# Kernel tuning notes

Measured on AMD Instinct MI355X. Metric: run time of the kernel, lower is better.

The kernel has to match this reference:

```python
import jax, jax.numpy as jnp
import numpy as np

B, N, D, K = 32, 1024, 64, 2


def _spatial_attention(x, w1, w2, vs, bs):
    # x: (B, N, D); matches SpatialAttention on x.unsqueeze(1) with c_in=1
    e1 = x @ w1                                   # (B, N)
    e2 = x @ w2                                   # (B, N)
    prod = e1[:, :, None] * e2[:, None, :]        # (B, N, N) outer product
    e = jnp.einsum('ij,bjk->bik', vs, jax.nn.sigmoid(prod + bs))
    return jax.nn.softmax(e, axis=-1)


def setup_inputs() -> dict:
    key = jax.random.key(0)
    ks = jax.random.split(key, 16)
    s = jnp.float32(1.0 / np.sqrt(N))  # kaiming-like scale for NxN params
    return {
        'x': jax.random.normal(ks[0], (B, N * D), jnp.float32),
        'x0': jax.random.normal(ks[1], (B, N, D), jnp.float32),
        'w': jnp.eye(D, dtype=jnp.float32) + 0.01 * jax.random.normal(ks[2], (D, D), jnp.float32),
        'd': jnp.ones((D,), jnp.float32),
        'alpha': 0.8 * jnp.ones((N,), jnp.float32),
        'f_w1': jax.random.uniform(ks[3], (D,), jnp.float32),
        'f_w2': jax.random.uniform(ks[4], (D,), jnp.float32),
        'f_vs': s * jax.random.normal(ks[5], (N, N), jnp.float32),
        'f_bs': s * jax.random.normal(ks[6], (N, N), jnp.float32),
        'g_w1': jax.random.uniform(ks[7], (D,), jnp.float32),
        'g_w2': jax.random.uniform(ks[8], (D,), jnp.float32),
        'g_vs': s * jax.random.normal(ks[9], (N, N), jnp.float32),
        'g_bs': s * jax.random.normal(ks[10], (N, N), jnp.float32),
        'conv_w': jax.random.normal(ks[11], (K,), jnp.float32) / np.sqrt(K),
        'conv_b': jnp.zeros((1,), jnp.float32),
        'adj_mx': s * jax.random.normal(ks[12], (K, N, N), jnp.float32),
    }


def reference(x, x0, w, d, alpha, f_w1, f_w2, f_vs, f_bs,
              g_w1, g_w2, g_vs, g_bs, conv_w, conv_b, adj_mx):
    xr = x.reshape(B, N, D)
    I_N = jnp.eye(N, dtype=x.dtype)

    # ---- F (drift) ----
    E = _spatial_attention(xr, f_w1, f_w2, f_vs, f_bs)      # (B, N, N)
    xe = jnp.einsum('bij,bjd->bid', E - I_N, xr)            # attention message passing
    # channel_conv(adj @ x): 1x1 conv over K Chebyshev channels == weighted sum + bias
    A_hat = adj_mx - I_N                                    # (K, N, N)
    A_mix = jnp.einsum('k,kij->ij', conv_w, A_hat)          # fold K into one (N, N)
    xa = jnp.einsum('ij,bjd->bid', A_mix, xr) + conv_b[0]
    dc = jnp.clip(d, 0.0, 1.0)
    W_hat = (w * dc) @ w.T - jnp.eye(D, dtype=x.dtype)
    xw = xr @ W_hat
    x0t = x0 * jax.nn.sigmoid(alpha)[None, :, None]
    f = jnp.tanh(xe + xa + xw + x0t).reshape(B, N * D)

    # ---- G (diffusion), uses E cached from F ----
    N_att = _spatial_attention(xr, g_w1, g_w2, g_vs, g_bs)  # (B, N, N)
    N_hat = N_att / (E + 1e-5)
    g = jnp.tanh(jnp.einsum('bij,bjd->bid', N_hat, xr)).reshape(B, N * D)

    return f, g
```

## Files before the change

kernel.cpp:

```cpp
#include <hip/hip_runtime.h>
#include <math.h>

constexpr int B_ = 32;
constexpr int N_ = 1024;
constexpr int D_ = 64;
constexpr int BCH = 16;

typedef short short8 __attribute__((ext_vector_type(8)));
typedef float f32x4 __attribute__((ext_vector_type(4)));
typedef int   int4_ __attribute__((ext_vector_type(4)));

__device__ __forceinline__ float sigf(float v) {
    return 1.0f / (1.0f + __expf(-v));
}
__device__ __forceinline__ unsigned short f2b(float f) {
    unsigned u = __float_as_uint(f);
    unsigned r = u + 0x7fffu + ((u >> 16) & 1u);
    return (unsigned short)(r >> 16);
}
__device__ __forceinline__ float b2f(unsigned int h) {
    return __uint_as_float(h << 16);
}
__device__ __forceinline__ unsigned pack4(int a, int b, int c, int d) {
    return (unsigned)(a & 255) | ((unsigned)(b & 255) << 8) |
           ((unsigned)(c & 255) << 16) | ((unsigned)(d & 255) << 24);
}

#define GLD16(gp, lp)                                                        \
    __builtin_amdgcn_global_load_lds(                                        \
        (const __attribute__((address_space(1))) unsigned int*)(const void*)(gp), \
        (__attribute__((address_space(3))) unsigned int*)(void*)(lp), 16, 0, 0)

__global__ void k_dots(const float* __restrict__ x,
                       const float* __restrict__ fw1, const float* __restrict__ fw2,
                       const float* __restrict__ gw1, const float* __restrict__ gw2,
                       const float* __restrict__ alpha,
                       float* __restrict__ e1f, float* __restrict__ e2f,
                       float* __restrict__ e1g, float* __restrict__ e2g,
                       float* __restrict__ sa)
{
    int t = blockIdx.x * blockDim.x + threadIdx.x;
    if (t < N_) sa[t] = sigf(alpha[t]);
    if (t >= B_ * N_) return;
    const float* xr = x + (size_t)t * D_;
    float s1 = 0.f, s2 = 0.f, s3 = 0.f, s4 = 0.f;
#pragma unroll 8
    for (int d = 0; d < D_; d++) {
        float v = xr[d];
        s1 += v * fw1[d];
        s2 += v * fw2[d];
        s3 += v * gw1[d];
        s4 += v * gw2[d];
    }
    e1f[t] = s1; e2f[t] = s2; e1g[t] = s3; e2g[t] = s4;
}

__global__ void k_what2_split(const float* __restrict__ w, const float* __restrict__ dvec,
                              unsigned short* __restrict__ W2h, unsigned short* __restrict__ W2l)
{
    int t = blockIdx.x * blockDim.x + threadIdx.x;
    if (t >= D_ * D_) return;
    int i = t / D_, j = t % D_;
    float s = 0.f;
    for (int q = 0; q < D_; q++) {
        float dc = fminf(fmaxf(dvec[q], 0.0f), 1.0f);
        s += w[i * D_ + q] * dc * w[j * D_ + q];
    }
    if (i == j) s -= 2.0f;
    unsigned short h = f2b(s);
    W2h[t] = h;
    W2l[t] = f2b(s - b2f(h));
}

__global__ void k_amix_split(const float* __restrict__ adj, const float* __restrict__ cw,
                             unsigned short* __restrict__ AmixH, unsigned short* __restrict__ AmixL)
{
    int t = blockIdx.x * blockDim.x + threadIdx.x;
    if (t >= N_ * N_) return;
    int i = t >> 10, j = t & (N_ - 1);
    float c0 = cw[0], c1 = cw[1];
    float v = c0 * adj[t] + c1 * adj[(size_t)N_ * N_ + t];
    if (i == j) v -= (c0 + c1);
    unsigned short h = f2b(v);
    AmixH[t] = h;
    AmixL[t] = f2b(v - b2f(h));
}

__global__ void k_zinit(unsigned* __restrict__ amaxbits)
{
    if (threadIdx.x < 2) amaxbits[threadIdx.x] = 0;
}

__global__ void k_amax(const float* __restrict__ fvs, const float* __restrict__ gvs,
                       unsigned* __restrict__ amaxbits)
{
    int fg = blockIdx.y;
    const float* src = fg ? gvs : fvs;
    int t = threadIdx.x;
    size_t base = ((size_t)blockIdx.x * 256 + t) * 16;
    float m = 0.f;
#pragma unroll
    for (int q = 0; q < 4; q++) {
        float4 v = *(const float4*)(src + base + q * 4);
        m = fmaxf(m, fmaxf(fmaxf(fabsf(v.x), fabsf(v.y)), fmaxf(fabsf(v.z), fabsf(v.w))));
    }
#pragma unroll
    for (int o = 32; o > 0; o >>= 1) m = fmaxf(m, __shfl_xor(m, o, 64));
    __shared__ float red[4];
    if ((t & 63) == 0) red[t >> 6] = m;
    __syncthreads();
    if (t == 0) {
        m = fmaxf(fmaxf(red[0], red[1]), fmaxf(red[2], red[3]));
        atomicMax(&amaxbits[fg], __float_as_uint(m));
    }
}

__launch_bounds__(256)
__global__ void k_aquant(const float* __restrict__ fvs, const float* __restrict__ gvs,
                         const float* __restrict__ amaxf,
                         signed char* __restrict__ AHf, signed char* __restrict__ ALf,
                         signed char* __restrict__ AHg, signed char* __restrict__ ALg,
                         float* __restrict__ rsumf, float* __restrict__ rsumg)
{
    int row = blockIdx.x;
    int fg  = blockIdx.y;
    const float* src = fg ? gvs : fvs;
    signed char* hp = fg ? AHg : AHf;
    signed char* lp = fg ? ALg : ALf;
    float* rs = fg ? rsumg : rsumf;
    float inv = 32512.f / amaxf[fg];
    int t = threadIdx.x;
    int j = t * 4;
    float4 v = *(const float4*)(src + (size_t)row * N_ + j);
    float a[4] = {v.x, v.y, v.z, v.w};
    int qh[4], ql[4], s = 0;
#pragma unroll
    for (int e = 0; e < 4; e++) {
        int q = __float2int_rn(a[e] * inv);
        q = min(max(q, -32512), 32512);
        int h = (q + 128) >> 8;
        qh[e] = h;
        ql[e] = q - (h << 8);
        s += q;
    }
    *(unsigned*)(hp + (size_t)row * N_ + j) = pack4(qh[0], qh[1], qh[2], qh[3]);
    *(unsigned*)(lp + (size_t)row * N_ + j) = pack4(ql[0], ql[1], ql[2], ql[3]);
#pragma unroll
    for (int o = 32; o > 0; o >>= 1) s += __shfl_xor(s, o, 64);
    __shared__ int red[4];
    if ((t & 63) == 0) red[t >> 6] = s;
    __syncthreads();
    if (t == 0) rs[row] = (float)(red[0] + red[1] + red[2] + red[3]);
}

__launch_bounds__(256)
__global__ void k_xt_split(const float* __restrict__ xc,
                           unsigned short* __restrict__ XTh, unsigned short* __restrict__ XTl)
{
    int j0 = blockIdx.x * 64;
    int bc = blockIdx.y;
    int t  = threadIdx.x;
    __shared__ float S_l[64][65];
    {
        int j = t >> 2, dc = (t & 3) * 16;
        const float* src = xc + ((size_t)bc * N_ + j0 + j) * D_ + dc;
#pragma unroll
        for (int q = 0; q < 4; q++) {
            float4 v = *(const float4*)(src + q * 4);
            S_l[j][dc + q * 4 + 0] = v.x;
            S_l[j][dc + q * 4 + 1] = v.y;
            S_l[j][dc + q * 4 + 2] = v.z;
            S_l[j][dc + q * 4 + 3] = v.w;
        }
    }
    __syncthreads();
    {
        int d = t >> 2, jc = (t & 3) * 16;
        unsigned short hs[16], ls[16];
#pragma unroll
        for (int u = 0; u < 16; u++) {
            float v = S_l[jc + u][d];
            hs[u] = f2b(v);
            ls[u] = f2b(v - b2f(hs[u]));
        }
        uint4 hv0, hv1, lv0, lv1;
        hv0.x = hs[0] | (hs[1] << 16);  hv0.y = hs[2] | (hs[3] << 16);
        hv0.z = hs[4] | (hs[5] << 16);  hv0.w = hs[6] | (hs[7] << 16);
        hv1.x = hs[8] | (hs[9] << 16);  hv1.y = hs[10] | (hs[11] << 16);
        hv1.z = hs[12] | (hs[13] << 16); hv1.w = hs[14] | (hs[15] << 16);
        lv0.x = ls[0] | (ls[1] << 16);  lv0.y = ls[2] | (ls[3] << 16);
        lv0.z = ls[4] | (ls[5] << 16);  lv0.w = ls[6] | (ls[7] << 16);
        lv1.x = ls[8] | (ls[9] << 16);  lv1.y = ls[10] | (ls[11] << 16);
        lv1.z = ls[12] | (ls[13] << 16); lv1.w = ls[14] | (ls[15] << 16);
        size_t base = ((size_t)bc * D_ + d) * N_ + j0 + jc;
        *(uint4*)(XTh + base) = hv0;  *(uint4*)(XTh + base + 8) = hv1;
        *(uint4*)(XTl + base) = lv0;  *(uint4*)(XTl + base + 8) = lv1;
    }
}

__launch_bounds__(256)
__global__ void k_sigsplit2(const float* __restrict__ fbs, const float* __restrict__ gbs,
                            const float* __restrict__ e1f_, const float* __restrict__ e2f_,
                            const float* __restrict__ e1g_, const float* __restrict__ e2g_,
                            signed char* __restrict__ SHf, signed char* __restrict__ SLf,
                            signed char* __restrict__ SHg, signed char* __restrict__ SLg)
{
    int j0 = blockIdx.x * 64;
    int k0 = blockIdx.y * 64;
    int z  = blockIdx.z;
    int b  = z & (BCH - 1);
    int fg = z / BCH;
    const float* bs = fg ? gbs : fbs;
    const float* e1 = fg ? e1g_ : e1f_;
    const float* e2 = fg ? e2g_ : e2f_;
    signed char* SH = fg ? SHg : SHf;
    signed char* SL = fg ? SLg : SLf;
    int t  = threadIdx.x;
    __shared__ float S_l[64][65];
    {
        int j  = t >> 2;
        int kc = (t & 3) * 16;
        float e1v = e1[(size_t)b * N_ + j0 + j];
#pragma unroll
        for (int q = 0; q < 4; q++) {
            float4 bsv = *(const float4*)(bs + (size_t)(j0 + j) * N_ + k0 + kc + q * 4);
            float4 e2v = *(const float4*)(e2 + (size_t)b * N_ + k0 + kc + q * 4);
            S_l[j][kc + q * 4 + 0] = sigf(fmaf(e1v, e2v.x, bsv.x));
            S_l[j][kc + q * 4 + 1] = sigf(fmaf(e1v, e2v.y, bsv.y));
            S_l[j][kc + q * 4 + 2] = sigf(fmaf(e1v, e2v.z, bsv.z));
            S_l[j][kc + q * 4 + 3] = sigf(fmaf(e1v, e2v.w, bsv.w));
        }
    }
    __syncthreads();
    {
        int k  = t >> 2;
        int jc = (t & 3) * 16;
        int hh[16], ll[16];
#pragma unroll
        for (int u = 0; u < 16; u++) {
            float v = S_l[jc + u][k];
            int q = __float2int_rn(v * 65024.f) - 32512;
            q = min(max(q, -32512), 32512);
            int h = (q + 128) >> 8;
            hh[u] = h;
            ll[u] = q - (h << 8);
        }
        uint4 H, L;
        H.x = pack4(hh[0], hh[1], hh[2], hh[3]);   H.y = pack4(hh[4], hh[5], hh[6], hh[7]);
        H.z = pack4(hh[8], hh[9], hh[10], hh[11]); H.w = pack4(hh[12], hh[13], hh[14], hh[15]);
        L.x = pack4(ll[0], ll[1], ll[2], ll[3]);   L.y = pack4(ll[4], ll[5], ll[6], ll[7]);
        L.z = pack4(ll[8], ll[9], ll[10], ll[11]); L.w = pack4(ll[12], ll[13], ll[14], ll[15]);
        size_t base = (size_t)(b * N_ + k0 + k) * N_ + j0 + jc;
        *(uint4*)(SH + base) = H;
        *(uint4*)(SL + base) = L;
    }
}

__launch_bounds__(256, 2)
__global__ void k_gemm2i(const signed char* __restrict__ AHf, const signed char* __restrict__ ALf,
                         const signed char* __restrict__ AHg, const signed char* __restrict__ ALg,
                         const signed char* __restrict__ SHf, const signed char* __restrict__ SLf,
                         const signed char* __restrict__ SHg, const signed char* __restrict__ SLg,
                         const float* __restrict__ rsumf, const float* __restrict__ rsumg,
                         const float* __restrict__ amaxf,
                         float* __restrict__ LF, float* __restrict__ LG)
{
    const int fg = blockIdx.z;
    const signed char* AH = fg ? AHg : AHf;
    const signed char* AL = fg ? ALg : ALf;
    const signed char* SH = fg ? SHg : SHf;
    const signed char* SL = fg ? SLg : SLf;
    const float* rsum = fg ? rsumg : rsumf;
    float* Lo = fg ? LG : LF;
    const float scale = amaxf[fg] * (1.0f / (32512.f * 65024.f));

    const int b  = blockIdx.y;
    const int i0 = (blockIdx.x >> 3) * 128;
    const int k0 = (blockIdx.x & 7) * 128;
    const int t    = threadIdx.x;
    const int lane = t & 63;
    const int wave = t >> 6;
    const int wr   = wave >> 1;
    const int wc   = wave & 1;
    const int quad = lane >> 4;
    const int m16  = lane & 15;

    __shared__ __align__(16) signed char lds[32768];
    signed char* AHl = lds;
    signed char* ALl = lds + 8192;
    signed char* BHl = lds + 16384;
    signed char* BLl = lds + 24576;

    const signed char* gsrc;
    signed char* ldst;
    int rowbase;
    if (wave == 0)      { gsrc = AH; ldst = AHl; rowbase = i0; }
    else if (wave == 1) { gsrc = AL; ldst = ALl; rowbase = i0; }
    else if (wave == 2) { gsrc = SH; ldst = BHl; rowbase = b * N_ + k0; }
    else                { gsrc = SL; ldst = BLl; rowbase = b * N_ + k0; }

    int4_ accm[4][4], accc[4][4];
#pragma unroll
    for (int mi = 0; mi < 4; mi++)
#pragma unroll
        for (int ni = 0; ni < 4; ni++) {
            accm[mi][ni] = (int4_){0, 0, 0, 0};
            accc[mi][ni] = (int4_){0, 0, 0, 0};
        }

    const int rr = lane >> 2;
    const int cc = lane & 3;
    const int gcq = cc ^ ((rr >> 1) & 3);
    const int rpos = (quad ^ ((m16 >> 1) & 3)) * 16;

    for (int step = 0; step < 16; step++) {
        const int jb = step * 64;
        __syncthreads();
#pragma unroll
        for (int it = 0; it < 8; it++) {
            int r = it * 16 + rr;
            const signed char* gp = gsrc + (size_t)(rowbase + r) * N_ + jb + gcq * 16;
            GLD16(gp, ldst + it * 1024);
        }
        __syncthreads();

        int4_ ah[4], al[4];
#pragma unroll
        for (int mi = 0; mi < 4; mi++) {
            int row = wr * 64 + mi * 16 + m16;
            ah[mi] = *(const int4_*)(AHl + row * 64 + rpos);
            al[mi] = *(const int4_*)(ALl + row * 64 + rpos);
        }
#pragma unroll
        for (int ni = 0; ni < 4; ni++) {
            int row = wc * 64 + ni * 16 + m16;
            int4_ bh = *(const int4_*)(BHl + row * 64 + rpos);
            int4_ bl = *(const int4_*)(BLl + row * 64 + rpos);
#pragma unroll
            for (int mi = 0; mi < 4; mi++) {
                accm[mi][ni] = __builtin_amdgcn_mfma_i32_16x16x64_i8(
                    ah[mi], bh, accm[mi][ni], 0, 0, 0);
                accc[mi][ni] = __builtin_amdgcn_mfma_i32_16x16x64_i8(
                    ah[mi], bl, accc[mi][ni], 0, 0, 0);
                accc[mi][ni] = __builtin_amdgcn_mfma_i32_16x16x64_i8(
                    al[mi], bh, accc[mi][ni], 0, 0, 0);
            }
        }
    }

#pragma unroll
    for (int mi = 0; mi < 4; mi++)
#pragma unroll
        for (int ni = 0; ni < 4; ni++) {
            int row = i0 + wr * 64 + mi * 16 + quad * 4;
            int col = k0 + wc * 64 + ni * 16 + m16;
            size_t base = ((size_t)b * N_ + row) * N_ + col;
#pragma unroll
            for (int r = 0; r < 4; r++) {
                float v = (65536.f * (float)accm[mi][ni][r] +
                           256.f * (float)accc[mi][ni][r] +
                           32512.f * rsum[row + r]) * scale;
                Lo[base + (size_t)r * N_] = v;
            }
        }
}

__launch_bounds__(256, 2)
__global__ void k_fused(const float* __restrict__ LF, const float* __restrict__ LG,
                        const unsigned short* __restrict__ AmixH, const unsigned short* __restrict__ AmixL,
                        const unsigned short* __restrict__ XTh, const unsigned short* __restrict__ XTl,
                        const unsigned short* __restrict__ W2h, const unsigned short* __restrict__ W2l,
                        const float* __restrict__ xc, const float* __restrict__ x0c,
                        const float* __restrict__ sa, const float* __restrict__ cb,
                        float* __restrict__ outf, float* __restrict__ outg)
{
    const int i0 = blockIdx.x * 32;
    const int bc = blockIdx.y;
    const int t    = threadIdx.x;
    const int lane = t & 63;
    const int wave = t >> 6;
    const int quad = lane >> 4;
    const int m16  = lane & 15;
    const int l7   = lane & 7;
    const int r_sub = lane >> 3;
    const int gc    = l7 ^ r_sub;

    __shared__ __align__(16) unsigned short lds[18432];
    unsigned short* E_l  = lds;
    unsigned short* Nh_l = lds + 2048;
    unsigned short* Nl_l = lds + 4096;
    unsigned short* Xh_l = lds + 6144;
    unsigned short* Xl_l = lds + 10240;
    unsigned short* Ah_l = lds + 14336;
    unsigned short* Al_l = lds + 16384;
    __shared__ float invf_l[32], invg_l[32];

    {
        int r  = t >> 3;
        int c0 = (t & 7) * 4;
        const float* lf = LF + ((size_t)bc * N_ + i0 + r) * N_;
        const float* lg = LG + ((size_t)bc * N_ + i0 + r) * N_;
        float sf = 0.f, sg = 0.f;
        for (int k = 0; k < 32; k++) {
            float4 a = *(const float4*)(lf + c0 + k * 32);
            float4 b = *(const float4*)(lg + c0 + k * 32);
            sf += __expf(a.x) + __expf(a.y) + __expf(a.z) + __expf(a.w);
            sg += __expf(b.x) + __expf(b.y) + __expf(b.z) + __expf(b.w);
        }
        sf += __shfl_xor(sf, 1, 64); sf += __shfl_xor(sf, 2, 64); sf += __shfl_xor(sf, 4, 64);
        sg += __shfl_xor(sg, 1, 64); sg += __shfl_xor(sg, 2, 64); sg += __shfl_xor(sg, 4, 64);
        if ((t & 7) == 0) { invf_l[r] = 1.f / sf; invg_l[r] = 1.f / sg; }
    }
    __syncthreads();

    f32x4 accf[2], accg[2];
#pragma unroll
    for (int u = 0; u < 2; u++) {
        accf[u] = (f32x4){0.f, 0.f, 0.f, 0.f};
        accg[u] = (f32x4){0.f, 0.f, 0.f, 0.f};
    }
    const int rowA = (wave & 1) * 16 + m16;
    const int cg0  = (wave >> 1) * 2;

    for (int step = 0; step < 16; step++) {
        const int jb = step * 64;
        __syncthreads();
        for (int i = 0; i < 6; i++) {
            int gi = wave * 6 + i;
            const unsigned short* gp;
            unsigned short* lp;
            if (gi < 8) {
                gp = XTh + ((size_t)bc * D_ + gi * 8 + r_sub) * N_ + jb + gc * 8;
                lp = Xh_l + gi * 512;
            } else if (gi < 16) {
                int g2 = gi - 8;
                gp = XTl + ((size_t)bc * D_ + g2 * 8 + r_sub) * N_ + jb + gc * 8;
                lp = Xl_l + g2 * 512;
            } else if (gi < 20) {
                int g2 = gi - 16;
                gp = AmixH + (size_t)(i0 + g2 * 8 + r_sub) * N_ + jb + gc * 8;
                lp = Ah_l + g2 * 512;
            } else {
                int g2 = gi - 20;
                gp = AmixL + (size_t)(i0 + g2 * 8 + r_sub) * N_ + jb + gc * 8;
                lp = Al_l + g2 * 512;
            }
            GLD16(gp, lp);
        }
        {
            int r  = t >> 3;
            int jc = (t & 7) * 8;
            const float* lf = LF + ((size_t)bc * N_ + i0 + r) * N_ + jb + jc;
            const float* lg = LG + ((size_t)bc * N_ + i0 + r) * N_ + jb + jc;
            float4 f0 = *(const float4*)lf;
            float4 f1 = *(const float4*)(lf + 4);
            float4 g0 = *(const float4*)lg;
            float4 g1 = *(const float4*)(lg + 4);
            float fa[8] = {f0.x, f0.y, f0.z, f0.w, f1.x, f1.y, f1.z, f1.w};
            float ga[8] = {g0.x, g0.y, g0.z, g0.w, g1.x, g1.y, g1.z, g1.w};
            float fi = invf_l[r], gi2 = invg_l[r];
            short8 ev, nhv, nlv;
#pragma unroll
            for (int e = 0; e < 8; e++) {
                float E = __expf(fa[e]) * fi;
                float nh = __expf(ga[e]) * gi2 / (E + 1e-5f);
                ev[e] = (short)f2b(E);
                unsigned short h = f2b(nh);
                nhv[e] = (short)h;
                nlv[e] = (short)f2b(nh - b2f(h));
            }
            int pos = (((jc >> 3) ^ (r & 7))) * 8;
            *(short8*)(E_l  + r * 64 + pos) = ev;
            *(short8*)(Nh_l + r * 64 + pos) = nhv;
            *(short8*)(Nl_l + r * 64 + pos) = nlv;
        }
        __syncthreads();
#pragma unroll
        for (int kc = 0; kc < 2; kc++) {
            const int ch = ((kc * 4 + quad) ^ l7) * 8;
            short8 e  = *(const short8*)(E_l  + rowA * 64 + ch);
            short8 ah = *(const short8*)(Ah_l + rowA * 64 + ch);
            short8 al = *(const short8*)(Al_l + rowA * 64 + ch);
            short8 nh = *(const short8*)(Nh_l + rowA * 64 + ch);
            short8 nl = *(const short8*)(Nl_l + rowA * 64 + ch);
#pragma unroll
            for (int u = 0; u < 2; u++) {
                int rowB = (cg0 + u) * 16 + m16;
                short8 bh = *(const short8*)(Xh_l + rowB * 64 + ch);
                short8 bl = *(const short8*)(Xl_l + rowB * 64 + ch);
                accf[u] = __builtin_amdgcn_mfma_f32_16x16x32_bf16(e,  bh, accf[u], 0, 0, 0);
                accf[u] = __builtin_amdgcn_mfma_f32_16x16x32_bf16(e,  bl, accf[u], 0, 0, 0);
                accf[u] = __builtin_amdgcn_mfma_f32_16x16x32_bf16(ah, bh, accf[u], 0, 0, 0);
                accf[u] = __builtin_amdgcn_mfma_f32_16x16x32_bf16(ah, bl, accf[u], 0, 0, 0);
                accf[u] = __builtin_amdgcn_mfma_f32_16x16x32_bf16(al, bh, accf[u], 0, 0, 0);
                accg[u] = __builtin_amdgcn_mfma_f32_16x16x32_bf16(nh, bh, accg[u], 0, 0, 0);
                accg[u] = __builtin_amdgcn_mfma_f32_16x16x32_bf16(nh, bl, accg[u], 0, 0, 0);
                accg[u] = __builtin_amdgcn_mfma_f32_16x16x32_bf16(nl, bh, accg[u], 0, 0, 0);
            }
        }
    }

    __syncthreads();
    {
        for (int i = 0; i < 4; i++) {
            int gi = wave * 4 + i;
            const unsigned short* gsrc2 = (gi < 8) ? W2h : W2l;
            int g2 = gi & 7;
            unsigned short* lp = ((gi < 8) ? Xh_l : Xl_l) + g2 * 512;
            GLD16(gsrc2 + (size_t)(g2 * 8 + r_sub) * 64 + gc * 8, lp);
        }
        int r  = t >> 3;
        int dc = (t & 7) * 8;
        const float* xrow = xc + ((size_t)bc * N_ + i0 + r) * D_ + dc;
        float4 v0 = *(const float4*)xrow;
        float4 v1 = *(const float4*)(xrow + 4);
        float vv[8] = {v0.x, v0.y, v0.z, v0.w, v1.x, v1.y, v1.z, v1.w};
        short8 hh, ll;
#pragma unroll
        for (int e = 0; e < 8; e++) {
            unsigned short h = f2b(vv[e]);
            hh[e] = (short)h;
            ll[e] = (short)f2b(vv[e] - b2f(h));
        }
        int pos = (((dc >> 3) ^ (r & 7))) * 8;
        *(short8*)(E_l  + r * 64 + pos) = hh;
        *(short8*)(Nh_l + r * 64 + pos) = ll;
    }
    __syncthreads();
#pragma unroll
    for (int kc = 0; kc < 2; kc++) {
        const int ch = ((kc * 4 + quad) ^ l7) * 8;
        short8 xh = *(const short8*)(E_l  + rowA * 64 + ch);
        short8 xl = *(const short8*)(Nh_l + rowA * 64 + ch);
#pragma unroll
        for (int u = 0; u < 2; u++) {
            int rowB = (cg0 + u) * 16 + m16;
            short8 bh = *(const short8*)(Xh_l + rowB * 64 + ch);
            short8 bl = *(const short8*)(Xl_l + rowB * 64 + ch);
            accf[u] = __builtin_amdgcn_mfma_f32_16x16x32_bf16(xh, bh, accf[u], 0, 0, 0);
            accf[u] = __builtin_amdgcn_mfma_f32_16x16x32_bf16(xh, bl, accf[u], 0, 0, 0);
            accf[u] = __builtin_amdgcn_mfma_f32_16x16x32_bf16(xl, bh, accf[u], 0, 0, 0);
        }
    }

    float cbv = cb[0];
#pragma unroll
    for (int u = 0; u < 2; u++) {
#pragma unroll
        for (int r = 0; r < 4; r++) {
            int row = i0 + (wave & 1) * 16 + quad * 4 + r;
            int col = (cg0 + u) * 16 + m16;
            size_t o = ((size_t)bc * N_ + row) * D_ + col;
            outf[o] = tanhf(accf[u][r] + x0c[o] * sa[row] + cbv);
            outg[o] = tanhf(accg[u][r]);
        }
    }
}

extern "C" void kernel_launch(void* const* d_in, const int* in_sizes, int n_in,
                              void* d_out, int out_size, void* d_ws, size_t ws_size,
                              hipStream_t stream)
{
    const float* x     = (const float*)d_in[0];
    const float* x0    = (const float*)d_in[1];
    const float* w     = (const float*)d_in[2];
    const float* dvec  = (const float*)d_in[3];
    const float* alpha = (const float*)d_in[4];
    const float* fw1   = (const float*)d_in[5];
    const float* fw2   = (const float*)d_in[6];
    const float* fvs   = (const float*)d_in[7];
    const float* fbs   = (const float*)d_in[8];
    const float* gw1   = (const float*)d_in[9];
    const float* gw2   = (const float*)d_in[10];
    const float* gvs   = (const float*)d_in[11];
    const float* gbs   = (const float*)d_in[12];
    const float* cw    = (const float*)d_in[13];
    const float* cb    = (const float*)d_in[14];
    const float* adj   = (const float*)d_in[15];

    float* outf = (float*)d_out;
    float* outg = outf + (size_t)B_ * N_ * D_;

    char* p = (char*)d_ws;
    auto alloc = [&](size_t bytes) { void* r = p; p += (bytes + 255) & ~(size_t)255; return r; };

    float* e1f = (float*)alloc(B_ * N_ * 4);
    float* e2f = (float*)alloc(B_ * N_ * 4);
    float* e1g = (float*)alloc(B_ * N_ * 4);
    float* e2g = (float*)alloc(B_ * N_ * 4);
    float* sa  = (float*)alloc(N_ * 4);
    unsigned short* W2h = (unsigned short*)alloc(D_ * D_ * 2);
    unsigned short* W2l = (unsigned short*)alloc(D_ * D_ * 2);
    float* amaxf = (float*)alloc(2 * 4);
    float* rsumf = (float*)alloc(N_ * 4);
    float* rsumg = (float*)alloc(N_ * 4);
    unsigned short* AmixH = (unsigned short*)alloc((size_t)N_ * N_ * 2);
    unsigned short* AmixL = (unsigned short*)alloc((size_t)N_ * N_ * 2);
    signed char* AHf = (signed char*)alloc((size_t)N_ * N_);
    signed char* ALf = (signed char*)alloc((size_t)N_ * N_);
    signed char* AHg = (signed char*)alloc((size_t)N_ * N_);
    signed char* ALg = (signed char*)alloc((size_t)N_ * N_);
    unsigned short* XTh = (unsigned short*)alloc((size_t)BCH * D_ * N_ * 2);
    unsigned short* XTl = (unsigned short*)alloc((size_t)BCH * D_ * N_ * 2);
    signed char* SHf = (signed char*)alloc((size_t)BCH * N_ * N_);
    signed char* SLf = (signed char*)alloc((size_t)BCH * N_ * N_);
    signed char* SHg = (signed char*)alloc((size_t)BCH * N_ * N_);
    signed char* SLg = (signed char*)alloc((size_t)BCH * N_ * N_);
    float* LF = (float*)alloc((size_t)BCH * N_ * N_ * 4);
    float* LG = (float*)alloc((size_t)BCH * N_ * N_ * 4);
    (void)ws_size; (void)in_sizes; (void)n_in; (void)out_size;

    k_zinit<<<dim3(1), 64, 0, stream>>>((unsigned*)amaxf);
    k_amax<<<dim3(256, 2), 256, 0, stream>>>(fvs, gvs, (unsigned*)amaxf);
    k_aquant<<<dim3(1024, 2), 256, 0, stream>>>(fvs, gvs, amaxf,
                                                AHf, ALf, AHg, ALg, rsumf, rsumg);
    k_dots<<<dim3((B_ * N_) / 256), 256, 0, stream>>>(x, fw1, fw2, gw1, gw2, alpha,
                                                      e1f, e2f, e1g, e2g, sa);
    k_what2_split<<<dim3(16), 256, 0, stream>>>(w, dvec, W2h, W2l);
    k_amix_split<<<dim3(N_ * N_ / 256), 256, 0, stream>>>(adj, cw, AmixH, AmixL);

    for (int c = 0; c < B_ / BCH; c++) {
        int boff = c * BCH;
        const float* xc  = x  + (size_t)boff * N_ * D_;
        const float* x0c = x0 + (size_t)boff * N_ * D_;
        k_xt_split<<<dim3(16, BCH), 256, 0, stream>>>(xc, XTh, XTl);
        k_sigsplit2<<<dim3(16, 16, BCH * 2), 256, 0, stream>>>(
            fbs, gbs, e1f + boff * N_, e2f + boff * N_,
            e1g + boff * N_, e2g + boff * N_, SHf, SLf, SHg, SLg);
        k_gemm2i<<<dim3(64, BCH, 2), 256, 0, stream>>>(
            AHf, ALf, AHg, ALg, SHf, SLf, SHg, SLg, rsumf, rsumg, amaxf, LF, LG);
        k_fused<<<dim3(32, BCH), 256, 0, stream>>>(
            LF, LG, AmixH, AmixL, XTh, XTl, W2h, W2l,
            xc, x0c, sa, cb,
            outf + (size_t)boff * N_ * D_, outg + (size_t)boff * N_ * D_);
    }
}
```

Measured before the change: 494.1 us.

## Fuse softmax row-sum into GEMM epilogue and reuse bias tile across batch

```diff
diff --git a/kernel.cpp b/kernel.cpp
--- a/kernel.cpp
+++ b/kernel.cpp
@@ -91,6 +91,13 @@
     if (threadIdx.x < 2) amaxbits[threadIdx.x] = 0;
 }
 
+__global__ void k_zrs(float* __restrict__ rsEF, float* __restrict__ rsEG)
+{
+    int t = blockIdx.x * blockDim.x + threadIdx.x;
+    rsEF[t] = 0.f;
+    rsEG[t] = 0.f;
+}
+
 __global__ void k_amax(const float* __restrict__ fvs, const float* __restrict__ gvs,
                        unsigned* __restrict__ amaxbits)
 {
@@ -207,38 +214,46 @@
 {
     int j0 = blockIdx.x * 64;
     int k0 = blockIdx.y * 64;
-    int z  = blockIdx.z;
-    int b  = z & (BCH - 1);
-    int fg = z / BCH;
+    int fg = blockIdx.z;
     const float* bs = fg ? gbs : fbs;
     const float* e1 = fg ? e1g_ : e1f_;
     const float* e2 = fg ? e2g_ : e2f_;
     signed char* SH = fg ? SHg : SHf;
     signed char* SL = fg ? SLg : SLf;
     int t  = threadIdx.x;
-    __shared__ float S_l[64][65];
+
+    __shared__ float bs_l[64][65];
+    __shared__ float e1_l[BCH][64];
+    __shared__ float e2_l[BCH][64];
+
     {
-        int j  = t >> 2;
-        int kc = (t & 3) * 16;
-        float e1v = e1[(size_t)b * N_ + j0 + j];
+        int j = t >> 2, kc = (t & 3) * 16;
 #pragma unroll
         for (int q = 0; q < 4; q++) {
-            float4 bsv = *(const float4*)(bs + (size_t)(j0 + j) * N_ + k0 + kc + q * 4);
-            float4 e2v = *(const float4*)(e2 + (size_t)b * N_ + k0 + kc + q * 4);
-            S_l[j][kc + q * 4 + 0] = sigf(fmaf(e1v, e2v.x, bsv.x));
-            S_l[j][kc + q * 4 + 1] = sigf(fmaf(e1v, e2v.y, bsv.y));
-            S_l[j][kc + q * 4 + 2] = sigf(fmaf(e1v, e2v.z, bsv.z));
-            S_l[j][kc + q * 4 + 3] = sigf(fmaf(e1v, e2v.w, bsv.w));
+            float4 v = *(const float4*)(bs + (size_t)(j0 + j) * N_ + k0 + kc + q * 4);
+            bs_l[j][kc + q * 4 + 0] = v.x;
+            bs_l[j][kc + q * 4 + 1] = v.y;
+            bs_l[j][kc + q * 4 + 2] = v.z;
+            bs_l[j][kc + q * 4 + 3] = v.w;
+        }
+#pragma unroll
+        for (int i = 0; i < 4; i++) {
+            int idx = t + i * 256;
+            int b = idx >> 6, jj = idx & 63;
+            e1_l[b][jj] = e1[(size_t)b * N_ + j0 + jj];
+            e2_l[b][jj] = e2[(size_t)b * N_ + k0 + jj];
         }
     }
     __syncthreads();
-    {
-        int k  = t >> 2;
-        int jc = (t & 3) * 16;
+
+    int k  = t >> 2;
+    int jc = (t & 3) * 16;
+    for (int b = 0; b < BCH; b++) {
+        float e2k = e2_l[b][k];
         int hh[16], ll[16];
 #pragma unroll
         for (int u = 0; u < 16; u++) {
-            float v = S_l[jc + u][k];
+            float v = sigf(fmaf(e1_l[b][jc + u], e2k, bs_l[jc + u][k]));
             int q = __float2int_rn(v * 65024.f) - 32512;
             q = min(max(q, -32512), 32512);
             int h = (q + 128) >> 8;
@@ -263,7 +278,8 @@
                          const signed char* __restrict__ SHg, const signed char* __restrict__ SLg,
                          const float* __restrict__ rsumf, const float* __restrict__ rsumg,
                          const float* __restrict__ amaxf,
-                         float* __restrict__ LF, float* __restrict__ LG)
+                         float* __restrict__ LF, float* __restrict__ LG,
+                         float* __restrict__ rsEF, float* __restrict__ rsEG)
 {
     const int fg = blockIdx.z;
     const signed char* AH = fg ? AHg : AHf;
@@ -271,7 +287,8 @@
     const signed char* SH = fg ? SHg : SHf;
     const signed char* SL = fg ? SLg : SLf;
     const float* rsum = fg ? rsumg : rsumf;
-    float* Lo = fg ? LG : LF;
+    float* Lo  = fg ? LG : LF;
+    float* rsE = fg ? rsEG : rsEF;
     const float scale = amaxf[fg] * (1.0f / (32512.f * 65024.f));
 
     const int b  = blockIdx.y;
@@ -348,6 +365,12 @@
         }
     }
 
+    float psum[4][4];
+#pragma unroll
+    for (int mi = 0; mi < 4; mi++)
+#pragma unroll
+        for (int r = 0; r < 4; r++) psum[mi][r] = 0.f;
+
 #pragma unroll
     for (int mi = 0; mi < 4; mi++)
 #pragma unroll
@@ -361,12 +384,30 @@
                            256.f * (float)accc[mi][ni][r] +
                            32512.f * rsum[row + r]) * scale;
                 Lo[base + (size_t)r * N_] = v;
+                psum[mi][r] += __expf(v);
             }
         }
+#pragma unroll
+    for (int off = 1; off <= 8; off <<= 1)
+#pragma unroll
+        for (int mi = 0; mi < 4; mi++)
+#pragma unroll
+            for (int r = 0; r < 4; r++)
+                psum[mi][r] += __shfl_xor(psum[mi][r], off, 16);
+    if (m16 == 0) {
+#pragma unroll
+        for (int mi = 0; mi < 4; mi++)
+#pragma unroll
+            for (int r = 0; r < 4; r++) {
+                int rowI = i0 + wr * 64 + mi * 16 + quad * 4 + r;
+                atomicAdd(&rsE[(size_t)b * N_ + rowI], psum[mi][r]);
+            }
+    }
 }
 
 __launch_bounds__(256, 2)
 __global__ void k_fused(const float* __restrict__ LF, const float* __restrict__ LG,
+                        const float* __restrict__ rsEF, const float* __restrict__ rsEG,
                         const unsigned short* __restrict__ AmixH, const unsigned short* __restrict__ AmixL,
                         const unsigned short* __restrict__ XTh, const unsigned short* __restrict__ XTl,
                         const unsigned short* __restrict__ W2h, const unsigned short* __restrict__ W2l,
@@ -395,23 +436,8 @@
     unsigned short* Al_l = lds + 16384;
     __shared__ float invf_l[32], invg_l[32];
 
-    {
-        int r  = t >> 3;
-        int c0 = (t & 7) * 4;
-        const float* lf = LF + ((size_t)bc * N_ + i0 + r) * N_;
-        const float* lg = LG + ((size_t)bc * N_ + i0 + r) * N_;
-        float sf = 0.f, sg = 0.f;
-        for (int k = 0; k < 32; k++) {
-            float4 a = *(const float4*)(lf + c0 + k * 32);
-            float4 b = *(const float4*)(lg + c0 + k * 32);
-            sf += __expf(a.x) + __expf(a.y) + __expf(a.z) + __expf(a.w);
-            sg += __expf(b.x) + __expf(b.y) + __expf(b.z) + __expf(b.w);
-        }
-        sf += __shfl_xor(sf, 1, 64); sf += __shfl_xor(sf, 2, 64); sf += __shfl_xor(sf, 4, 64);
-        sg += __shfl_xor(sg, 1, 64); sg += __shfl_xor(sg, 2, 64); sg += __shfl_xor(sg, 4, 64);
-        if ((t & 7) == 0) { invf_l[r] = 1.f / sf; invg_l[r] = 1.f / sg; }
-    }
-    __syncthreads();
+    if (t < 32)       invf_l[t]      = 1.0f / rsEF[(size_t)bc * N_ + i0 + t];
+    else if (t < 64)  invg_l[t - 32] = 1.0f / rsEG[(size_t)bc * N_ + i0 + (t - 32)];
 
     f32x4 accf[2], accg[2];
 #pragma unroll
@@ -594,6 +620,8 @@
     float* amaxf = (float*)alloc(2 * 4);
     float* rsumf = (float*)alloc(N_ * 4);
     float* rsumg = (float*)alloc(N_ * 4);
+    float* rsEF  = (float*)alloc((size_t)BCH * N_ * 4);
+    float* rsEG  = (float*)alloc((size_t)BCH * N_ * 4);
     unsigned short* AmixH = (unsigned short*)alloc((size_t)N_ * N_ * 2);
     unsigned short* AmixL = (unsigned short*)alloc((size_t)N_ * N_ * 2);
     signed char* AHf = (signed char*)alloc((size_t)N_ * N_);
@@ -623,14 +651,16 @@
         int boff = c * BCH;
         const float* xc  = x  + (size_t)boff * N_ * D_;
         const float* x0c = x0 + (size_t)boff * N_ * D_;
+        k_zrs<<<dim3(BCH * N_ / 256), 256, 0, stream>>>(rsEF, rsEG);
         k_xt_split<<<dim3(16, BCH), 256, 0, stream>>>(xc, XTh, XTl);
-        k_sigsplit2<<<dim3(16, 16, BCH * 2), 256, 0, stream>>>(
+        k_sigsplit2<<<dim3(16, 16, 2), 256, 0, stream>>>(
             fbs, gbs, e1f + boff * N_, e2f + boff * N_,
             e1g + boff * N_, e2g + boff * N_, SHf, SLf, SHg, SLg);
         k_gemm2i<<<dim3(64, BCH, 2), 256, 0, stream>>>(
-            AHf, ALf, AHg, ALg, SHf, SLf, SHg, SLg, rsumf, rsumg, amaxf, LF, LG);
+            AHf, ALf, AHg, ALg, SHf, SLf, SHg, SLg, rsumf, rsumg, amaxf,
+            LF, LG, rsEF, rsEG);
         k_fused<<<dim3(32, BCH), 256, 0, stream>>>(
-            LF, LG, AmixH, AmixL, XTh, XTl, W2h, W2l,
+            LF, LG, rsEF, rsEG, AmixH, AmixL, XTh, XTl, W2h, W2l,
             xc, x0c, sa, cb,
             outf + (size_t)boff * N_ * D_, outg + (size_t)boff * N_ * D_);
     }
```

Result: no change. 499.0 us (+1.0%).
